# Performance work log

Measured on AMD Instinct MI355X. Metric: run time of the kernel, lower is better.

The kernel has to match this reference:

```python
import jax, jax.numpy as jnp
import numpy as np

D_MODEL = 1024
N_HEADS = 16
HEAD_DIM = D_MODEL // N_HEADS
WINDOW = 256


def setup_inputs() -> dict:
    key = jax.random.key(0)
    kx, kq, ko = jax.random.split(key, 3)
    B, T = 4, 2048
    x = jax.random.normal(kx, (B, T, D_MODEL), dtype=jnp.float32)
    s = 1.0 / np.sqrt(D_MODEL)
    w_qkv = jax.random.normal(kq, (D_MODEL, 3 * D_MODEL), dtype=jnp.float32) * s
    w_out = jax.random.normal(ko, (D_MODEL, D_MODEL), dtype=jnp.float32) * s
    return {"x": x, "w_qkv": w_qkv, "w_out": w_out}


def reference(x, w_qkv, w_out):
    B, T, C = x.shape
    qkv = (x @ w_qkv).reshape(B, T, 3, N_HEADS, HEAD_DIM)
    q, k, v = qkv[:, :, 0], qkv[:, :, 1], qkv[:, :, 2]  # [B,T,H,D]
    # sliding-window causal mask: position i attends to j in (i-W, i]
    i = jnp.arange(T)[:, None]
    j = jnp.arange(T)[None, :]
    allowed = (j <= i) & (j > i - WINDOW)
    mask = jnp.where(allowed, 0.0, -jnp.inf).astype(x.dtype)  # [T,T]
    scale = 1.0 / np.sqrt(HEAD_DIM)
    scores = jnp.einsum('bqhd,bkhd->bhqk', q, k) * scale + mask
    attn = jax.nn.softmax(scores, axis=-1)
    out = jnp.einsum('bhqk,bkhd->bqhd', attn, v).reshape(B, T, C)
    return out @ w_out
```

## Files before the change

### kernel.cpp

```cpp
#include <hip/hip_runtime.h>

typedef unsigned short u16;
typedef __attribute__((ext_vector_type(8))) short bh8;
typedef __attribute__((ext_vector_type(4))) float f4;
typedef __attribute__((ext_vector_type(4))) unsigned short us4;

#define T_SEQ 2048
#define NHEADS 16
#define DHEAD 64
#define WIN 256

__device__ __forceinline__ float bf2f(u16 u) {
  union { unsigned int i; float f; } v; v.i = ((unsigned int)u) << 16; return v.f;
}
__device__ __forceinline__ u16 f2bf(float f) {
  unsigned int u = __float_as_uint(f);
  u = u + 0x7fffu + ((u >> 16) & 1u);
  return (u16)(u >> 16);
}
__device__ __forceinline__ void async16(const void* g, void* l) {
  void* gv = const_cast<void*>(g);
  __builtin_amdgcn_global_load_lds(
      (__attribute__((address_space(1))) void*)gv,
      (__attribute__((address_space(3))) void*)l, 16, 0, 0);
}

__device__ __forceinline__ int is_f32_probe(const void* x) {
  const float* xf = (const float*)x;
  const int lane = threadIdx.x & 63;
  int bad = 0;
  #pragma unroll
  for (int u = 0; u < 4; ++u) {
    const float v = xf[lane * 4 + u];
    const float a = fabsf(v);
    bad |= (!(a < 64.f)) || (!(v == 0.f || a > 1e-30f));
  }
  return __any(bad) ? 0 : 1;
}

__global__ __launch_bounds__(256) void prep(
    const void* __restrict__ x, const void* __restrict__ w_qkv,
    const void* __restrict__ w_out, u16* __restrict__ xbf,
    u16* __restrict__ wqkvT, u16* __restrict__ woutT, int have_x)
{
  const int bid = blockIdx.x;
  const int tid = threadIdx.x;
  const int isf = is_f32_probe(x);

  if (bid < 4096) {
    if (!have_x) return;
    const size_t e = ((size_t)bid * 256 + tid) * 8;
    if (isf) {
      const float* f = (const float*)x;
      us4 o0, o1;
      #pragma unroll
      for (int u = 0; u < 4; ++u) { o0[u] = f2bf(f[e + u]); o1[u] = f2bf(f[e + 4 + u]); }
      *(us4*)&xbf[e] = o0; *(us4*)&xbf[e + 4] = o1;
    } else {
      *(us4*)&xbf[e]     = *(const us4*)&((const u16*)x)[e];
      *(us4*)&xbf[e + 4] = *(const us4*)&((const u16*)x)[e + 4];
    }
  } else {
    __shared__ alignas(16) u16 tile[32][33];
    const void* in; u16* out; int C, bx, by;
    if (bid < 4096 + 3072) { const int t = bid - 4096; in = w_qkv; out = wqkvT; C = 3072; bx = t % 96; by = t / 96; }
    else                   { const int t = bid - 7168; in = w_out; out = woutT; C = 1024; bx = t % 32; by = t / 32; }
    const int R = 1024;
    const int tx = tid & 31, ty = tid >> 5;
    const int xg = bx * 32 + tx;
    const int y0 = by * 32;
    #pragma unroll
    for (int i = ty; i < 32; i += 8) {
      u16 v;
      if (isf) v = f2bf(((const float*)in)[(size_t)(y0 + i) * C + xg]);
      else     v = ((const u16*)in)[(size_t)(y0 + i) * C + xg];
      tile[i][tx] = v;
    }
    __syncthreads();
    const int ox  = y0 + tx;
    const int oy0 = bx * 32;
    #pragma unroll
    for (int i = ty; i < 32; i += 8)
      out[(size_t)(oy0 + i) * R + ox] = tile[tx][i];
  }
}

template<bool ADYN, bool CDYN>
__global__ __launch_bounds__(256, 4) void gemm_bt(
    const void* __restrict__ A, const u16* __restrict__ Bt,
    void* __restrict__ C, int N, int K, int lda, int ldc,
    const void* __restrict__ xprobe)
{
  __shared__ alignas(16) u16 As[128 * 64];
  __shared__ alignas(16) u16 Bs[128 * 64];

  const int isf  = (ADYN || CDYN) ? is_f32_probe(xprobe) : 0;
  const int tid  = threadIdx.x;
  const int lane = tid & 63;
  const int w    = tid >> 6;
  const int wm   = (w >> 1) * 64;
  const int wn   = (w & 1) * 64;
  const int quad = lane >> 4;
  const int l16  = lane & 15;
  const int row0 = blockIdx.y * 128;
  const int col0 = blockIdx.x * 128;

  f4 acc[4][4] = {};

  size_t aoff[4]; const u16* bsrc[4]; int lofs[4];
  #pragma unroll
  for (int s = 0; s < 4; ++s) {
    const int r  = s * 32 + (tid >> 3);
    const int gc = (tid & 7) ^ (r & 7);
    aoff[s] = (size_t)(row0 + r) * lda + gc * 8;
    bsrc[s] = Bt + (size_t)(col0 + r) * K + gc * 8;
    lofs[s] = s * 4096 + tid * 16;
  }

  const bool af32 = ADYN && isf;

  for (int k0 = 0; k0 < K; k0 += 64) {
    if (af32) {
      const float* Af = (const float*)A;
      bh8 a[4];
      #pragma unroll
      for (int s = 0; s < 4; ++s) {
        f4 u0 = *(const f4*)(Af + aoff[s] + k0);
        f4 u1 = *(const f4*)(Af + aoff[s] + k0 + 4);
        #pragma unroll
        for (int u = 0; u < 4; ++u) { a[s][u] = (short)f2bf(u0[u]); a[s][u + 4] = (short)f2bf(u1[u]); }
      }
      __syncthreads();
      #pragma unroll
      for (int s = 0; s < 4; ++s) {
        *(bh8*)((char*)As + lofs[s]) = a[s];
        async16(bsrc[s] + k0, (char*)Bs + lofs[s]);
      }
    } else {
      const u16* A16 = (const u16*)A;
      __syncthreads();
      #pragma unroll
      for (int s = 0; s < 4; ++s) {
        async16(A16 + aoff[s] + k0, (char*)As + lofs[s]);
        async16(bsrc[s] + k0,       (char*)Bs + lofs[s]);
      }
    }
    __builtin_amdgcn_s_waitcnt(0);
    __syncthreads();

    #pragma unroll
    for (int ks = 0; ks < 2; ++ks) {
      bh8 af[4], bf[4];
      #pragma unroll
      for (int i = 0; i < 4; ++i) {
        const int row = wm + i * 16 + l16;
        const int lc  = (ks * 4 + quad) ^ (row & 7);
        af[i] = *(const bh8*)(As + row * 64 + lc * 8);
      }
      #pragma unroll
      for (int j = 0; j < 4; ++j) {
        const int row = wn + j * 16 + l16;
        const int lc  = (ks * 4 + quad) ^ (row & 7);
        bf[j] = *(const bh8*)(Bs + row * 64 + lc * 8);
      }
      #pragma unroll
      for (int i = 0; i < 4; ++i)
        #pragma unroll
        for (int j = 0; j < 4; ++j)
          acc[i][j] = __builtin_amdgcn_mfma_f32_16x16x32_bf16(af[i], bf[j], acc[i][j], 0, 0, 0);
    }
  }

  const bool cf32 = CDYN && isf;
  #pragma unroll
  for (int i = 0; i < 4; ++i) {
    #pragma unroll
    for (int j = 0; j < 4; ++j) {
      const int rb = row0 + wm + i * 16 + quad * 4;
      const int cc = col0 + wn + j * 16 + l16;
      #pragma unroll
      for (int r = 0; r < 4; ++r) {
        if (cf32) ((float*)C)[(size_t)(rb + r) * ldc + cc] = acc[i][j][r];
        else      ((u16*)C)[(size_t)(rb + r) * ldc + cc]   = f2bf(acc[i][j][r]);
      }
    }
  }
}

__global__ __launch_bounds__(256) void attn_mfma(const u16* __restrict__ qkv,
                                                 u16* __restrict__ att, int ldo)
{
  __shared__ alignas(16) u16 Kt[64 * 72];
  __shared__ alignas(16) u16 Vt[64 * 72];
  __shared__ alignas(16) u16 Ps[64 * 72];

  const int tid  = threadIdx.x;
  const int lane = tid & 63;
  const int w    = tid >> 6;
  const int quad = lane >> 4;
  const int l16  = lane & 15;
  const int qb = blockIdx.x, h = blockIdx.y, b = blockIdx.z;
  const int qs = qb * 64;

  const u16* base = qkv + (size_t)b * T_SEQ * 3072 + h * 64;

  const size_t qrowg = (size_t)(qs + w * 16 + l16) * 3072;
  bh8 qa0 = *(const bh8*)&base[qrowg + quad * 8];
  bh8 qa1 = *(const bh8*)&base[qrowg + 32 + quad * 8];
  #pragma unroll
  for (int u = 0; u < 8; ++u) {
    qa0[u] = (short)f2bf(bf2f((u16)qa0[u]) * 0.125f);
    qa1[u] = (short)f2bf(bf2f((u16)qa1[u]) * 0.125f);
  }

  f4 Oc[4] = {};
  float mst[4] = {-1e30f, -1e30f, -1e30f, -1e30f};
  float lst[4] = {0.f, 0.f, 0.f, 0.f};

  const int tmin = (qb >= 4) ? 0 : (4 - qb);
  const int c8  = (tid & 7) * 8;
  const int r0s = tid >> 3;

  for (int t = tmin; t < 5; ++t) {
    const int kt0 = qs - 256 + t * 64;
    const bool diag  = (t == 4);
    const bool ledge = (t == 0);
    const int kb_lo = ledge ? w : 0;
    const int kb_hi = diag  ? w : 3;
    __syncthreads();

    #pragma unroll
    for (int r = r0s; r < 64; r += 32) {
      *(bh8*)&Kt[r * 72 + c8] =
          *(const bh8*)&base[(size_t)(kt0 + r) * 3072 + 1024 + c8];
      bh8 v = *(const bh8*)&base[(size_t)(kt0 + r) * 3072 + 2048 + c8];
      const int kc = r >> 3, ki = r & 7;
      #pragma unroll
      for (int u = 0; u < 8; ++u) {
        const int d = c8 + u;
        Vt[d * 72 + ((kc ^ (d >> 3)) << 3) + ki] = (u16)v[u];
      }
    }
    __syncthreads();

    f4 S[4];
    #pragma unroll
    for (int kb = 0; kb < 4; ++kb) {
      if (kb < kb_lo || kb > kb_hi) {
        S[kb][0] = S[kb][1] = S[kb][2] = S[kb][3] = -1e30f;
      } else {
        const int krow = (kb * 16 + l16) * 72;
        bh8 kf0 = *(const bh8*)&Kt[krow + quad * 8];
        bh8 kf1 = *(const bh8*)&Kt[krow + 32 + quad * 8];
        f4 s = {};
        s = __builtin_amdgcn_mfma_f32_16x16x32_bf16(qa0, kf0, s, 0, 0, 0);
        s = __builtin_amdgcn_mfma_f32_16x16x32_bf16(qa1, kf1, s, 0, 0, 0);
        S[kb] = s;
      }
    }

    if (diag || ledge) {
      #pragma unroll
      for (int kb = 0; kb < 4; ++kb) {
        if (kb == w) {
          #pragma unroll
          for (int rr = 0; rr < 4; ++rr) {
            const int ii = quad * 4 + rr;
            const bool ok = diag ? (l16 <= ii) : (l16 > ii);
            if (!ok) S[kb][rr] = -1e30f;
          }
        }
      }
    }

    float tmax[4] = {-1e30f, -1e30f, -1e30f, -1e30f};
    #pragma unroll
    for (int kb = 0; kb < 4; ++kb)
      #pragma unroll
      for (int rr = 0; rr < 4; ++rr)
        tmax[rr] = fmaxf(tmax[rr], S[kb][rr]);
    #pragma unroll
    for (int off = 1; off < 16; off <<= 1)
      #pragma unroll
      for (int rr = 0; rr < 4; ++rr)
        tmax[rr] = fmaxf(tmax[rr], __shfl_xor(tmax[rr], off));

    const bool grew = (tmax[0] > mst[0] + 8.f) || (tmax[1] > mst[1] + 8.f) ||
                      (tmax[2] > mst[2] + 8.f) || (tmax[3] > mst[3] + 8.f);
    if (__any(grew)) {
      #pragma unroll
      for (int rr = 0; rr < 4; ++rr) {
        const float mnew = fmaxf(mst[rr], tmax[rr]);
        const float al = __expf(mst[rr] - mnew);
        mst[rr] = mnew;
        lst[rr] *= al;
        #pragma unroll
        for (int db = 0; db < 4; ++db) Oc[db][rr] *= al;
      }
    }

    float rsum[4] = {0.f, 0.f, 0.f, 0.f};
    const int swq = quad >> 1;
    #pragma unroll
    for (int kb = 0; kb < 4; ++kb) {
      const int kc = kb * 2 + (l16 >> 3);
      const int ki = l16 & 7;
      #pragma unroll
      for (int rr = 0; rr < 4; ++rr) {
        const float p = __expf(S[kb][rr] - mst[rr]);
        rsum[rr] += p;
        const int q = w * 16 + quad * 4 + rr;
        Ps[q * 72 + ((kc ^ swq) << 3) + ki] = f2bf(p);
      }
    }
    #pragma unroll
    for (int off = 1; off < 16; off <<= 1)
      #pragma unroll
      for (int rr = 0; rr < 4; ++rr)
        rsum[rr] += __shfl_xor(rsum[rr], off);
    #pragma unroll
    for (int rr = 0; rr < 4; ++rr)
      lst[rr] += rsum[rr];

    {
      const int q = w * 16 + l16;
      const int sw = (q >> 3) & 1;
      bh8 pa0 = *(const bh8*)&Ps[q * 72 + (((0 + quad) ^ sw) << 3)];
      bh8 pa1 = *(const bh8*)&Ps[q * 72 + (((4 + quad) ^ sw) << 3)];
      #pragma unroll
      for (int db = 0; db < 4; ++db) {
        const int d = db * 16 + l16;
        const int dsw = d >> 3;
        bh8 vb0 = *(const bh8*)&Vt[d * 72 + (((0 + quad) ^ dsw) << 3)];
        bh8 vb1 = *(const bh8*)&Vt[d * 72 + (((4 + quad) ^ dsw) << 3)];
        Oc[db] = __builtin_amdgcn_mfma_f32_16x16x32_bf16(pa0, vb0, Oc[db], 0, 0, 0);
        Oc[db] = __builtin_amdgcn_mfma_f32_16x16x32_bf16(pa1, vb1, Oc[db], 0, 0, 0);
      }
    }
  }

  u16* obase = att + (size_t)b * T_SEQ * ldo + h * 64;
  #pragma unroll
  for (int rr = 0; rr < 4; ++rr) {
    const int i = qs + w * 16 + quad * 4 + rr;
    const float inv = 1.f / lst[rr];
    #pragma unroll
    for (int db = 0; db < 4; ++db)
      obase[(size_t)i * ldo + db * 16 + l16] = f2bf(Oc[db][rr] * inv);
  }
}

extern "C" void kernel_launch(void* const* d_in, const int* in_sizes, int n_in,
                              void* d_out, int out_size, void* d_ws, size_t ws_size,
                              hipStream_t stream) {
  const void* x     = d_in[0];
  const void* w_qkv = d_in[1];
  const void* w_out = d_in[2];

  const size_t SZ_QKV = (size_t)8192 * 3072 * 2;
  const size_t SZ_XBF = (size_t)8192 * 1024 * 2;
  const size_t SZ_WQ  = (size_t)3072 * 1024 * 2;
  const size_t SZ_WO  = (size_t)1024 * 1024 * 2;
  const size_t SZ_ATT = (size_t)8192 * 1024 * 2;

  char* p = (char*)d_ws;
  u16* qkv   = (u16*)p; p += SZ_QKV;
  u16* wqkvT = (u16*)p; p += SZ_WQ;
  u16* woutT = (u16*)p; p += SZ_WO;
  u16* xbf   = (u16*)p; p += SZ_XBF;
  u16* attb  = (u16*)p;
  const size_t need_x   = SZ_QKV + SZ_WQ + SZ_WO + SZ_XBF;
  const bool have_x   = ws_size >= need_x;
  const bool have_att = ws_size >= need_x + SZ_ATT;

  prep<<<dim3(8192), 256, 0, stream>>>(x, w_qkv, w_out, xbf, wqkvT, woutT,
                                       have_x ? 1 : 0);

  if (have_x) {
    gemm_bt<false, false><<<dim3(24, 64), 256, 0, stream>>>(
        xbf, wqkvT, qkv, 3072, 1024, 1024, 3072, x);
  } else {
    gemm_bt<true, false><<<dim3(24, 64), 256, 0, stream>>>(
        x, wqkvT, qkv, 3072, 1024, 1024, 3072, x);
  }

  u16* attp  = have_att ? attb : qkv;
  const int ldo = have_att ? 1024 : 3072;
  attn_mfma<<<dim3(32, NHEADS, 4), 256, 0, stream>>>(qkv, attp, ldo);

  gemm_bt<false, true><<<dim3(8, 64), 256, 0, stream>>>(
      attp, woutT, d_out, 1024, 1024, ldo, 1024, x);
}
```

Measured before the change: 226.6 us.

## Add single-pass windowed attention kernel with pre-transposed V and GEMM tile swizzle

```diff
diff --git a/kernel.cpp b/kernel.cpp
--- a/kernel.cpp
+++ b/kernel.cpp
@@ -9,6 +9,8 @@
 #define NHEADS 16
 #define DHEAD 64
 #define WIN 256
+
+#define MF(a, b, c) __builtin_amdgcn_mfma_f32_16x16x32_bf16((a), (b), (c), 0, 0, 0)
 
 __device__ __forceinline__ float bf2f(u16 u) {
   union { unsigned int i; float f; } v; v.i = ((unsigned int)u) << 16; return v.f;
@@ -102,8 +104,18 @@
   const int wn   = (w & 1) * 64;
   const int quad = lane >> 4;
   const int l16  = lane & 15;
-  const int row0 = blockIdx.y * 128;
-  const int col0 = blockIdx.x * 128;
+
+  int bx = blockIdx.x, by = blockIdx.y;
+  {
+    const int nx = gridDim.x, nwg = nx * gridDim.y;
+    if ((nwg & 7) == 0) {
+      const int lin = by * nx + bx;
+      const int sw  = (lin & 7) * (nwg >> 3) + (lin >> 3);
+      bx = sw % nx; by = sw / nx;
+    }
+  }
+  const int row0 = by * 128;
+  const int col0 = bx * 128;
 
   f4 acc[4][4] = {};
 
@@ -167,7 +179,7 @@
       for (int i = 0; i < 4; ++i)
         #pragma unroll
         for (int j = 0; j < 4; ++j)
-          acc[i][j] = __builtin_amdgcn_mfma_f32_16x16x32_bf16(af[i], bf[j], acc[i][j], 0, 0, 0);
+          acc[i][j] = MF(af[i], bf[j], acc[i][j]);
     }
   }
 
@@ -184,6 +196,169 @@
         else      ((u16*)C)[(size_t)(rb + r) * ldc + cc]   = f2bf(acc[i][j][r]);
       }
     }
+  }
+}
+
+__global__ __launch_bounds__(256) void vtrans(const u16* __restrict__ qkv,
+                                              u16* __restrict__ vT)
+{
+  __shared__ alignas(16) u16 tile[32][33];
+  const int tid = threadIdx.x;
+  const int bh = blockIdx.z;
+  const int b = bh >> 4, h = bh & 15;
+  const int k0 = blockIdx.x * 32, d0 = blockIdx.y * 32;
+  const int tx = tid & 31, ty = tid >> 5;
+  const u16* src = qkv + (size_t)b * T_SEQ * 3072 + 2048 + h * 64;
+  #pragma unroll
+  for (int i = ty; i < 32; i += 8)
+    tile[i][tx] = src[(size_t)(k0 + i) * 3072 + d0 + tx];
+  __syncthreads();
+  u16* dst = vT + ((size_t)bh * 64 + d0) * T_SEQ + k0;
+  #pragma unroll
+  for (int i = ty; i < 32; i += 8)
+    dst[(size_t)i * T_SEQ + tx] = tile[tx][i];
+}
+
+__global__ __launch_bounds__(512) void attn_win(const u16* __restrict__ qkv,
+                                                const u16* __restrict__ vT,
+                                                u16* __restrict__ att, int ldo)
+{
+  __shared__ alignas(16) u16 Kt[384 * 64];
+  __shared__ alignas(16) u16 Vt[64 * 384];
+  __shared__ alignas(16) u16 Ps[8 * 16 * 72];
+
+  const int tid  = threadIdx.x;
+  const int lane = tid & 63;
+  const int w    = tid >> 6;
+  const int quad = lane >> 4;
+  const int l16  = lane & 15;
+  const int qb = blockIdx.x, h = blockIdx.y, b = blockIdx.z;
+  const int qs = qb * 128;
+  const int kbase = qs - 256;
+
+  const u16* base = qkv + (size_t)b * T_SEQ * 3072 + h * 64;
+  const u16* vTbh = vT + (size_t)(b * NHEADS + h) * 64 * T_SEQ;
+
+  #pragma unroll
+  for (int s = 0; s < 6; ++s) {
+    const int id = s * 512 + tid;
+    const int r  = id >> 3;
+    const int gc = (id & 7) ^ (r & 7);
+    int gk = kbase + r; gk = gk < 0 ? 0 : gk;
+    async16(&base[(size_t)gk * 3072 + 1024 + gc * 8], (char*)Kt + id * 16);
+  }
+  #pragma unroll
+  for (int s = 0; s < 6; ++s) {
+    const int id = s * 512 + tid;
+    const int d  = id / 48;
+    const int c  = id - d * 48;
+    const int gc = c ^ (d & 7);
+    int gk = kbase + gc * 8; gk = gk < 0 ? 0 : gk;
+    async16(vTbh + (size_t)d * T_SEQ + gk, (char*)Vt + id * 16);
+  }
+
+  const int q0w = qs + w * 16;
+  const size_t qrowg = (size_t)(q0w + l16) * 3072;
+  bh8 qa0 = *(const bh8*)&base[qrowg + quad * 8];
+  bh8 qa1 = *(const bh8*)&base[qrowg + 32 + quad * 8];
+  #pragma unroll
+  for (int u = 0; u < 8; ++u) {
+    qa0[u] = (short)f2bf(bf2f((u16)qa0[u]) * 0.125f);
+    qa1[u] = (short)f2bf(bf2f((u16)qa1[u]) * 0.125f);
+  }
+
+  __builtin_amdgcn_s_waitcnt(0);
+  __syncthreads();
+
+  const int qw16 = (qs >> 4) + w;
+  const int t_lo = qw16 >= 16 ? 0 : 16 - qw16;
+  const bool has_ledge = (t_lo == 0);
+
+  f4 S[17];
+  __builtin_amdgcn_s_setprio(1);
+  #pragma unroll
+  for (int t = 0; t < 17; ++t) {
+    if (t >= t_lo) {
+      const int kr = 16 * (w + t) + l16;
+      const int sw = l16 & 7;
+      bh8 kf0 = *(const bh8*)&Kt[kr * 64 + ((quad    ) ^ sw) * 8];
+      bh8 kf1 = *(const bh8*)&Kt[kr * 64 + ((quad + 4) ^ sw) * 8];
+      f4 s = {};
+      s = MF(qa0, kf0, s);
+      s = MF(qa1, kf1, s);
+      S[t] = s;
+    }
+  }
+  __builtin_amdgcn_s_setprio(0);
+
+  #pragma unroll
+  for (int rr = 0; rr < 4; ++rr) {
+    const int ii = quad * 4 + rr;
+    if (l16 > ii) S[16][rr] = -1e30f;
+    if (has_ledge && l16 <= ii) S[0][rr] = -1e30f;
+  }
+
+  float rsum[4] = {0.f, 0.f, 0.f, 0.f};
+  #pragma unroll
+  for (int t = 0; t < 17; ++t) {
+    if (t >= t_lo) {
+      #pragma unroll
+      for (int rr = 0; rr < 4; ++rr) {
+        const float p = __expf(S[t][rr]);
+        S[t][rr] = p;
+        rsum[rr] += p;
+      }
+    }
+  }
+  #pragma unroll
+  for (int off = 1; off < 16; off <<= 1)
+    #pragma unroll
+    for (int rr = 0; rr < 4; ++rr)
+      rsum[rr] += __shfl_xor(rsum[rr], off);
+
+  u16* Psw = Ps + w * 16 * 72;
+  f4 Oc[4] = {};
+  const int swq = quad >> 1;
+  const int swp = (l16 >> 3) & 1;
+  #pragma unroll
+  for (int g = 0; g < 5; ++g) {
+    if (4 * g + 3 < t_lo && g != 4) continue;
+    #pragma unroll
+    for (int kb = 0; kb < 4; ++kb) {
+      const int t = 4 * g + kb;
+      const int kc = kb * 2 + (l16 >> 3);
+      const int ki = l16 & 7;
+      #pragma unroll
+      for (int rr = 0; rr < 4; ++rr) {
+        const int qloc = quad * 4 + rr;
+        const u16 pv = (t <= 16 && t >= t_lo) ? f2bf(S[t][rr]) : (u16)0;
+        Psw[qloc * 72 + ((kc ^ swq) << 3) + ki] = pv;
+      }
+    }
+    bh8 pa0 = *(const bh8*)&Psw[l16 * 72 + (((0 + quad) ^ swp) << 3)];
+    bh8 pa1 = *(const bh8*)&Psw[l16 * 72 + (((4 + quad) ^ swp) << 3)];
+    __builtin_amdgcn_s_setprio(1);
+    #pragma unroll
+    for (int db = 0; db < 4; ++db) {
+      const int d = db * 16 + l16;
+      int cc0 = 2 * w + 8 * g + quad;     cc0 = cc0 > 47 ? 47 : cc0;
+      int cc1 = 2 * w + 8 * g + quad + 4; cc1 = cc1 > 47 ? 47 : cc1;
+      bh8 vb0 = *(const bh8*)&Vt[d * 384 + (cc0 ^ (d & 7)) * 8];
+      bh8 vb1 = *(const bh8*)&Vt[d * 384 + (cc1 ^ (d & 7)) * 8];
+      Oc[db] = MF(pa0, vb0, Oc[db]);
+      Oc[db] = MF(pa1, vb1, Oc[db]);
+    }
+    __builtin_amdgcn_s_setprio(0);
+  }
+
+  u16* obase = att + (size_t)b * T_SEQ * ldo + h * 64;
+  #pragma unroll
+  for (int rr = 0; rr < 4; ++rr) {
+    const int i = q0w + quad * 4 + rr;
+    const float inv = 1.f / rsum[rr];
+    #pragma unroll
+    for (int db = 0; db < 4; ++db)
+      obase[(size_t)i * ldo + db * 16 + l16] = f2bf(Oc[db][rr] * inv);
   }
 }
 
@@ -253,8 +428,8 @@
         bh8 kf0 = *(const bh8*)&Kt[krow + quad * 8];
         bh8 kf1 = *(const bh8*)&Kt[krow + 32 + quad * 8];
         f4 s = {};
-        s = __builtin_amdgcn_mfma_f32_16x16x32_bf16(qa0, kf0, s, 0, 0, 0);
-        s = __builtin_amdgcn_mfma_f32_16x16x32_bf16(qa1, kf1, s, 0, 0, 0);
+        s = MF(qa0, kf0, s);
+        s = MF(qa1, kf1, s);
         S[kb] = s;
       }
     }
@@ -324,17 +499,17 @@
 
     {
       const int q = w * 16 + l16;
-      const int sw = (q >> 3) & 1;
-      bh8 pa0 = *(const bh8*)&Ps[q * 72 + (((0 + quad) ^ sw) << 3)];
-      bh8 pa1 = *(const bh8*)&Ps[q * 72 + (((4 + quad) ^ sw) << 3)];
+      const int swp = (q >> 3) & 1;
+      bh8 pa0 = *(const bh8*)&Ps[q * 72 + (((0 + quad) ^ swp) << 3)];
+      bh8 pa1 = *(const bh8*)&Ps[q * 72 + (((4 + quad) ^ swp) << 3)];
       #pragma unroll
       for (int db = 0; db < 4; ++db) {
         const int d = db * 16 + l16;
         const int dsw = d >> 3;
         bh8 vb0 = *(const bh8*)&Vt[d * 72 + (((0 + quad) ^ dsw) << 3)];
         bh8 vb1 = *(const bh8*)&Vt[d * 72 + (((4 + quad) ^ dsw) << 3)];
-        Oc[db] = __builtin_amdgcn_mfma_f32_16x16x32_bf16(pa0, vb0, Oc[db], 0, 0, 0);
-        Oc[db] = __builtin_amdgcn_mfma_f32_16x16x32_bf16(pa1, vb1, Oc[db], 0, 0, 0);
+        Oc[db] = MF(pa0, vb0, Oc[db]);
+        Oc[db] = MF(pa1, vb1, Oc[db]);
       }
     }
   }
@@ -361,6 +536,7 @@
   const size_t SZ_XBF = (size_t)8192 * 1024 * 2;
   const size_t SZ_WQ  = (size_t)3072 * 1024 * 2;
   const size_t SZ_WO  = (size_t)1024 * 1024 * 2;
+  const size_t SZ_VT  = (size_t)64 * 64 * 2048 * 2;
   const size_t SZ_ATT = (size_t)8192 * 1024 * 2;
 
   char* p = (char*)d_ws;
@@ -368,10 +544,12 @@
   u16* wqkvT = (u16*)p; p += SZ_WQ;
   u16* woutT = (u16*)p; p += SZ_WO;
   u16* xbf   = (u16*)p; p += SZ_XBF;
+  u16* vTb   = (u16*)p; p += SZ_VT;
   u16* attb  = (u16*)p;
-  const size_t need_x   = SZ_QKV + SZ_WQ + SZ_WO + SZ_XBF;
-  const bool have_x   = ws_size >= need_x;
-  const bool have_att = ws_size >= need_x + SZ_ATT;
+  const size_t need_x  = SZ_QKV + SZ_WQ + SZ_WO + SZ_XBF;
+  const bool have_x    = ws_size >= need_x;
+  const bool have_vt   = ws_size >= need_x + SZ_VT;
+  const bool have_att  = ws_size >= need_x + SZ_VT + SZ_ATT;
 
   prep<<<dim3(8192), 256, 0, stream>>>(x, w_qkv, w_out, xbf, wqkvT, woutT,
                                        have_x ? 1 : 0);
@@ -384,9 +562,14 @@
         x, wqkvT, qkv, 3072, 1024, 1024, 3072, x);
   }
 
-  u16* attp  = have_att ? attb : qkv;
+  u16* attp = have_att ? attb : qkv;
   const int ldo = have_att ? 1024 : 3072;
-  attn_mfma<<<dim3(32, NHEADS, 4), 256, 0, stream>>>(qkv, attp, ldo);
+  if (have_vt) {
+    vtrans<<<dim3(64, 2, 64), 256, 0, stream>>>(qkv, vTb);
+    attn_win<<<dim3(16, NHEADS, 4), 512, 0, stream>>>(qkv, vTb, attp, ldo);
+  } else {
+    attn_mfma<<<dim3(32, NHEADS, 4), 256, 0, stream>>>(qkv, attp, ldo);
+  }
 
   gemm_bt<false, true><<<dim3(8, 64), 256, 0, stream>>>(
       attp, woutT, d_out, 1024, 1024, ldo, 1024, x);
```

After: 232.3 us. 1.03x slower.

## Fuse all stages into one persistent kernel with grid barriers

Applied to the files above, without the earlier changes.

```diff
diff --git a/kernel.cpp b/kernel.cpp
--- a/kernel.cpp
+++ b/kernel.cpp
@@ -9,6 +9,9 @@
 #define NHEADS 16
 #define DHEAD 64
 #define WIN 256
+#define NBLK 512
+
+#define MF(a, b, c) __builtin_amdgcn_mfma_f32_16x16x32_bf16((a), (b), (c), 0, 0, 0)
 
 __device__ __forceinline__ float bf2f(u16 u) {
   union { unsigned int i; float f; } v; v.i = ((unsigned int)u) << 16; return v.f;
@@ -36,6 +39,327 @@
     bad |= (!(a < 64.f)) || (!(v == 0.f || a > 1e-30f));
   }
   return __any(bad) ? 0 : 1;
+}
+
+__device__ __forceinline__ void gridbar(unsigned int* bar, unsigned int target) {
+  __syncthreads();
+  if (threadIdx.x == 0) {
+    __hip_atomic_fetch_add(bar, 1u, __ATOMIC_ACQ_REL, __HIP_MEMORY_SCOPE_AGENT);
+    while (__hip_atomic_load(bar, __ATOMIC_ACQUIRE, __HIP_MEMORY_SCOPE_AGENT) < target) {
+      __builtin_amdgcn_s_sleep(8);
+    }
+  }
+  __syncthreads();
+  __threadfence();
+}
+
+__device__ __forceinline__ void gtile(
+    const u16* __restrict__ A, const u16* __restrict__ Bt, void* __restrict__ C,
+    int K, int lda, int ldc, int row0, int col0, bool cf32,
+    u16* As, u16* Bs)
+{
+  const int tid  = threadIdx.x;
+  const int lane = tid & 63;
+  const int w    = tid >> 6;
+  const int wm   = (w >> 1) * 64;
+  const int wn   = (w & 1) * 64;
+  const int quad = lane >> 4;
+  const int l16  = lane & 15;
+
+  f4 acc[4][4] = {};
+
+  size_t aoff[4]; const u16* bsrc[4]; int lofs[4];
+  #pragma unroll
+  for (int s = 0; s < 4; ++s) {
+    const int r  = s * 32 + (tid >> 3);
+    const int gc = (tid & 7) ^ (r & 7);
+    aoff[s] = (size_t)(row0 + r) * lda + gc * 8;
+    bsrc[s] = Bt + (size_t)(col0 + r) * K + gc * 8;
+    lofs[s] = s * 4096 + tid * 16;
+  }
+
+  for (int k0 = 0; k0 < K; k0 += 64) {
+    __syncthreads();
+    #pragma unroll
+    for (int s = 0; s < 4; ++s) {
+      async16(A + aoff[s] + k0, (char*)As + lofs[s]);
+      async16(bsrc[s] + k0,     (char*)Bs + lofs[s]);
+    }
+    __builtin_amdgcn_s_waitcnt(0);
+    __syncthreads();
+
+    #pragma unroll
+    for (int ks = 0; ks < 2; ++ks) {
+      bh8 af[4], bf[4];
+      #pragma unroll
+      for (int i = 0; i < 4; ++i) {
+        const int row = wm + i * 16 + l16;
+        const int lc  = (ks * 4 + quad) ^ (row & 7);
+        af[i] = *(const bh8*)(As + row * 64 + lc * 8);
+      }
+      #pragma unroll
+      for (int j = 0; j < 4; ++j) {
+        const int row = wn + j * 16 + l16;
+        const int lc  = (ks * 4 + quad) ^ (row & 7);
+        bf[j] = *(const bh8*)(Bs + row * 64 + lc * 8);
+      }
+      #pragma unroll
+      for (int i = 0; i < 4; ++i)
+        #pragma unroll
+        for (int j = 0; j < 4; ++j)
+          acc[i][j] = MF(af[i], bf[j], acc[i][j]);
+    }
+  }
+  __syncthreads();
+
+  #pragma unroll
+  for (int i = 0; i < 4; ++i) {
+    #pragma unroll
+    for (int j = 0; j < 4; ++j) {
+      const int rb = row0 + wm + i * 16 + quad * 4;
+      const int cc = col0 + wn + j * 16 + l16;
+      #pragma unroll
+      for (int r = 0; r < 4; ++r) {
+        if (cf32) ((float*)C)[(size_t)(rb + r) * ldc + cc] = acc[i][j][r];
+        else      ((u16*)C)[(size_t)(rb + r) * ldc + cc]   = f2bf(acc[i][j][r]);
+      }
+    }
+  }
+}
+
+__device__ __forceinline__ void attn_vb(
+    const u16* __restrict__ qkv, u16* __restrict__ att, int ldo,
+    int qb, int h, int b, u16* Kt, u16* Vt, u16* Ps)
+{
+  const int tid  = threadIdx.x;
+  const int lane = tid & 63;
+  const int w    = tid >> 6;
+  const int quad = lane >> 4;
+  const int l16  = lane & 15;
+  const int qs = qb * 64;
+
+  const u16* base = qkv + (size_t)b * T_SEQ * 3072 + h * 64;
+
+  const size_t qrowg = (size_t)(qs + w * 16 + l16) * 3072;
+  bh8 qa0 = *(const bh8*)&base[qrowg + quad * 8];
+  bh8 qa1 = *(const bh8*)&base[qrowg + 32 + quad * 8];
+  #pragma unroll
+  for (int u = 0; u < 8; ++u) {
+    qa0[u] = (short)f2bf(bf2f((u16)qa0[u]) * 0.125f);
+    qa1[u] = (short)f2bf(bf2f((u16)qa1[u]) * 0.125f);
+  }
+
+  f4 Oc[4] = {};
+  float mst[4] = {-1e30f, -1e30f, -1e30f, -1e30f};
+  float lst[4] = {0.f, 0.f, 0.f, 0.f};
+
+  const int tmin = (qb >= 4) ? 0 : (4 - qb);
+  const int c8  = (tid & 7) * 8;
+  const int r0s = tid >> 3;
+
+  for (int t = tmin; t < 5; ++t) {
+    const int kt0 = qs - 256 + t * 64;
+    const bool diag  = (t == 4);
+    const bool ledge = (t == 0);
+    const int kb_lo = ledge ? w : 0;
+    const int kb_hi = diag  ? w : 3;
+    __syncthreads();
+
+    #pragma unroll
+    for (int r = r0s; r < 64; r += 32) {
+      *(bh8*)&Kt[r * 72 + c8] =
+          *(const bh8*)&base[(size_t)(kt0 + r) * 3072 + 1024 + c8];
+      bh8 v = *(const bh8*)&base[(size_t)(kt0 + r) * 3072 + 2048 + c8];
+      const int kc = r >> 3, ki = r & 7;
+      #pragma unroll
+      for (int u = 0; u < 8; ++u) {
+        const int d = c8 + u;
+        Vt[d * 72 + ((kc ^ (d >> 3)) << 3) + ki] = (u16)v[u];
+      }
+    }
+    __syncthreads();
+
+    f4 S[4];
+    #pragma unroll
+    for (int kb = 0; kb < 4; ++kb) {
+      if (kb < kb_lo || kb > kb_hi) {
+        S[kb][0] = S[kb][1] = S[kb][2] = S[kb][3] = -1e30f;
+      } else {
+        const int krow = (kb * 16 + l16) * 72;
+        bh8 kf0 = *(const bh8*)&Kt[krow + quad * 8];
+        bh8 kf1 = *(const bh8*)&Kt[krow + 32 + quad * 8];
+        f4 s = {};
+        s = MF(qa0, kf0, s);
+        s = MF(qa1, kf1, s);
+        S[kb] = s;
+      }
+    }
+
+    if (diag || ledge) {
+      #pragma unroll
+      for (int kb = 0; kb < 4; ++kb) {
+        if (kb == w) {
+          #pragma unroll
+          for (int rr = 0; rr < 4; ++rr) {
+            const int ii = quad * 4 + rr;
+            const bool ok = diag ? (l16 <= ii) : (l16 > ii);
+            if (!ok) S[kb][rr] = -1e30f;
+          }
+        }
+      }
+    }
+
+    float tmax[4] = {-1e30f, -1e30f, -1e30f, -1e30f};
+    #pragma unroll
+    for (int kb = 0; kb < 4; ++kb)
+      #pragma unroll
+      for (int rr = 0; rr < 4; ++rr)
+        tmax[rr] = fmaxf(tmax[rr], S[kb][rr]);
+    #pragma unroll
+    for (int off = 1; off < 16; off <<= 1)
+      #pragma unroll
+      for (int rr = 0; rr < 4; ++rr)
+        tmax[rr] = fmaxf(tmax[rr], __shfl_xor(tmax[rr], off));
+
+    const bool grew = (tmax[0] > mst[0] + 8.f) || (tmax[1] > mst[1] + 8.f) ||
+                      (tmax[2] > mst[2] + 8.f) || (tmax[3] > mst[3] + 8.f);
+    if (__any(grew)) {
+      #pragma unroll
+      for (int rr = 0; rr < 4; ++rr) {
+        const float mnew = fmaxf(mst[rr], tmax[rr]);
+        const float al = __expf(mst[rr] - mnew);
+        mst[rr] = mnew;
+        lst[rr] *= al;
+        #pragma unroll
+        for (int db = 0; db < 4; ++db) Oc[db][rr] *= al;
+      }
+    }
+
+    float rsum[4] = {0.f, 0.f, 0.f, 0.f};
+    const int swq = quad >> 1;
+    #pragma unroll
+    for (int kb = 0; kb < 4; ++kb) {
+      const int kc = kb * 2 + (l16 >> 3);
+      const int ki = l16 & 7;
+      #pragma unroll
+      for (int rr = 0; rr < 4; ++rr) {
+        const float p = __expf(S[kb][rr] - mst[rr]);
+        rsum[rr] += p;
+        const int q = w * 16 + quad * 4 + rr;
+        Ps[q * 72 + ((kc ^ swq) << 3) + ki] = f2bf(p);
+      }
+    }
+    #pragma unroll
+    for (int off = 1; off < 16; off <<= 1)
+      #pragma unroll
+      for (int rr = 0; rr < 4; ++rr)
+        rsum[rr] += __shfl_xor(rsum[rr], off);
+    #pragma unroll
+    for (int rr = 0; rr < 4; ++rr)
+      lst[rr] += rsum[rr];
+
+    {
+      const int q = w * 16 + l16;
+      const int swp = (q >> 3) & 1;
+      bh8 pa0 = *(const bh8*)&Ps[q * 72 + (((0 + quad) ^ swp) << 3)];
+      bh8 pa1 = *(const bh8*)&Ps[q * 72 + (((4 + quad) ^ swp) << 3)];
+      #pragma unroll
+      for (int db = 0; db < 4; ++db) {
+        const int d = db * 16 + l16;
+        const int dsw = d >> 3;
+        bh8 vb0 = *(const bh8*)&Vt[d * 72 + (((0 + quad) ^ dsw) << 3)];
+        bh8 vb1 = *(const bh8*)&Vt[d * 72 + (((4 + quad) ^ dsw) << 3)];
+        Oc[db] = MF(pa0, vb0, Oc[db]);
+        Oc[db] = MF(pa1, vb1, Oc[db]);
+      }
+    }
+  }
+  __syncthreads();
+
+  u16* obase = att + (size_t)b * T_SEQ * ldo + h * 64;
+  #pragma unroll
+  for (int rr = 0; rr < 4; ++rr) {
+    const int i = qs + w * 16 + quad * 4 + rr;
+    const float inv = 1.f / lst[rr];
+    #pragma unroll
+    for (int db = 0; db < 4; ++db)
+      obase[(size_t)i * ldo + db * 16 + l16] = f2bf(Oc[db][rr] * inv);
+  }
+}
+
+__global__ __launch_bounds__(256, 2) void fused(
+    const void* __restrict__ x, const void* __restrict__ w_qkv,
+    const void* __restrict__ w_out, void* __restrict__ out,
+    u16* __restrict__ xbf, u16* __restrict__ wqkvT, u16* __restrict__ woutT,
+    u16* __restrict__ qkv, u16* __restrict__ attb, unsigned int* bar)
+{
+  __shared__ alignas(16) u16 smem[2 * 128 * 64];
+  const int bid = blockIdx.x;
+  const int tid = threadIdx.x;
+  const int isf = is_f32_probe(x);
+
+  #pragma unroll
+  for (int i = 0; i < 8; ++i) {
+    const size_t e = (((size_t)(bid * 8 + i)) * 256 + tid) * 8;
+    if (isf) {
+      const float* f = (const float*)x;
+      us4 o0, o1;
+      #pragma unroll
+      for (int u = 0; u < 4; ++u) { o0[u] = f2bf(f[e + u]); o1[u] = f2bf(f[e + 4 + u]); }
+      *(us4*)&xbf[e] = o0; *(us4*)&xbf[e + 4] = o1;
+    } else {
+      *(us4*)&xbf[e]     = *(const us4*)&((const u16*)x)[e];
+      *(us4*)&xbf[e + 4] = *(const us4*)&((const u16*)x)[e + 4];
+    }
+  }
+  {
+    u16 (*tile)[33] = (u16(*)[33])smem;
+    const int tx4 = (tid & 7) * 4;
+    const int iy  = tid >> 3;
+    for (int i = 0; i < 8; ++i) {
+      const int j = bid * 8 + i;
+      const void* in; u16* outw; int C, bx, by;
+      if (j < 3072) { in = w_qkv; outw = wqkvT; C = 3072; bx = j % 96; by = j / 96; }
+      else          { const int t = j - 3072; in = w_out; outw = woutT; C = 1024; bx = t % 32; by = t / 32; }
+      const int y0 = by * 32;
+      __syncthreads();
+      if (isf) {
+        f4 v = *(const f4*)&((const float*)in)[(size_t)(y0 + iy) * C + bx * 32 + tx4];
+        #pragma unroll
+        for (int u = 0; u < 4; ++u) tile[iy][tx4 + u] = f2bf(v[u]);
+      } else {
+        us4 v = *(const us4*)&((const u16*)in)[(size_t)(y0 + iy) * C + bx * 32 + tx4];
+        #pragma unroll
+        for (int u = 0; u < 4; ++u) tile[iy][tx4 + u] = v[u];
+      }
+      __syncthreads();
+      const int i2 = tid >> 3;
+      us4 o;
+      #pragma unroll
+      for (int u = 0; u < 4; ++u) o[u] = tile[tx4 + u][i2];
+      *(us4*)&outw[(size_t)(bx * 32 + i2) * 1024 + y0 + tx4] = o;
+    }
+  }
+  gridbar(bar, NBLK);
+
+  #pragma unroll
+  for (int i = 0; i < 3; ++i) {
+    const int t = bid + NBLK * i;
+    gtile(xbf, wqkvT, qkv, 1024, 1024, 3072,
+          (t / 24) * 128, (t % 24) * 128, false, smem, smem + 8192);
+  }
+  gridbar(bar, 2 * NBLK);
+
+  #pragma unroll
+  for (int i = 0; i < 4; ++i) {
+    const int t = bid + NBLK * i;
+    attn_vb(qkv, attb, 1024, t & 31, (t >> 5) & 15, t >> 9,
+            smem, smem + 4608, smem + 9216);
+  }
+  gridbar(bar, 3 * NBLK);
+
+  gtile(attb, woutT, out, 1024, 1024, 1024,
+        (bid / 8) * 128, (bid % 8) * 128, isf != 0, smem, smem + 8192);
 }
 
 __global__ __launch_bounds__(256) void prep(
@@ -65,23 +389,24 @@
     const void* in; u16* out; int C, bx, by;
     if (bid < 4096 + 3072) { const int t = bid - 4096; in = w_qkv; out = wqkvT; C = 3072; bx = t % 96; by = t / 96; }
     else                   { const int t = bid - 7168; in = w_out; out = woutT; C = 1024; bx = t % 32; by = t / 32; }
-    const int R = 1024;
-    const int tx = tid & 31, ty = tid >> 5;
-    const int xg = bx * 32 + tx;
+    const int tx4 = (tid & 7) * 4;
+    const int iy  = tid >> 3;
     const int y0 = by * 32;
-    #pragma unroll
-    for (int i = ty; i < 32; i += 8) {
-      u16 v;
-      if (isf) v = f2bf(((const float*)in)[(size_t)(y0 + i) * C + xg]);
-      else     v = ((const u16*)in)[(size_t)(y0 + i) * C + xg];
-      tile[i][tx] = v;
+    if (isf) {
+      f4 v = *(const f4*)&((const float*)in)[(size_t)(y0 + iy) * C + bx * 32 + tx4];
+      #pragma unroll
+      for (int u = 0; u < 4; ++u) tile[iy][tx4 + u] = f2bf(v[u]);
+    } else {
+      us4 v = *(const us4*)&((const u16*)in)[(size_t)(y0 + iy) * C + bx * 32 + tx4];
+      #pragma unroll
+      for (int u = 0; u < 4; ++u) tile[iy][tx4 + u] = v[u];
     }
     __syncthreads();
-    const int ox  = y0 + tx;
-    const int oy0 = bx * 32;
-    #pragma unroll
-    for (int i = ty; i < 32; i += 8)
-      out[(size_t)(oy0 + i) * R + ox] = tile[tx][i];
+    const int i2 = tid >> 3;
+    us4 o;
+    #pragma unroll
+    for (int u = 0; u < 4; ++u) o[u] = tile[tx4 + u][i2];
+    *(us4*)&out[(size_t)(bx * 32 + i2) * 1024 + y0 + tx4] = o;
   }
 }
 
@@ -167,7 +492,7 @@
       for (int i = 0; i < 4; ++i)
         #pragma unroll
         for (int j = 0; j < 4; ++j)
-          acc[i][j] = __builtin_amdgcn_mfma_f32_16x16x32_bf16(af[i], bf[j], acc[i][j], 0, 0, 0);
+          acc[i][j] = MF(af[i], bf[j], acc[i][j]);
     }
   }
 
@@ -187,167 +512,13 @@
   }
 }
 
-__global__ __launch_bounds__(256) void attn_mfma(const u16* __restrict__ qkv,
-                                                 u16* __restrict__ att, int ldo)
+__global__ __launch_bounds__(256) void attn_legacy(const u16* __restrict__ qkv,
+                                                   u16* __restrict__ att, int ldo)
 {
   __shared__ alignas(16) u16 Kt[64 * 72];
   __shared__ alignas(16) u16 Vt[64 * 72];
   __shared__ alignas(16) u16 Ps[64 * 72];
-
-  const int tid  = threadIdx.x;
-  const int lane = tid & 63;
-  const int w    = tid >> 6;
-  const int quad = lane >> 4;
-  const int l16  = lane & 15;
-  const int qb = blockIdx.x, h = blockIdx.y, b = blockIdx.z;
-  const int qs = qb * 64;
-
-  const u16* base = qkv + (size_t)b * T_SEQ * 3072 + h * 64;
-
-  const size_t qrowg = (size_t)(qs + w * 16 + l16) * 3072;
-  bh8 qa0 = *(const bh8*)&base[qrowg + quad * 8];
-  bh8 qa1 = *(const bh8*)&base[qrowg + 32 + quad * 8];
-  #pragma unroll
-  for (int u = 0; u < 8; ++u) {
-    qa0[u] = (short)f2bf(bf2f((u16)qa0[u]) * 0.125f);
-    qa1[u] = (short)f2bf(bf2f((u16)qa1[u]) * 0.125f);
-  }
-
-  f4 Oc[4] = {};
-  float mst[4] = {-1e30f, -1e30f, -1e30f, -1e30f};
-  float lst[4] = {0.f, 0.f, 0.f, 0.f};
-
-  const int tmin = (qb >= 4) ? 0 : (4 - qb);
-  const int c8  = (tid & 7) * 8;
-  const int r0s = tid >> 3;
-
-  for (int t = tmin; t < 5; ++t) {
-    const int kt0 = qs - 256 + t * 64;
-    const bool diag  = (t == 4);
-    const bool ledge = (t == 0);
-    const int kb_lo = ledge ? w : 0;
-    const int kb_hi = diag  ? w : 3;
-    __syncthreads();
-
-    #pragma unroll
-    for (int r = r0s; r < 64; r += 32) {
-      *(bh8*)&Kt[r * 72 + c8] =
-          *(const bh8*)&base[(size_t)(kt0 + r) * 3072 + 1024 + c8];
-      bh8 v = *(const bh8*)&base[(size_t)(kt0 + r) * 3072 + 2048 + c8];
-      const int kc = r >> 3, ki = r & 7;
-      #pragma unroll
-      for (int u = 0; u < 8; ++u) {
-        const int d = c8 + u;
-        Vt[d * 72 + ((kc ^ (d >> 3)) << 3) + ki] = (u16)v[u];
-      }
-    }
-    __syncthreads();
-
-    f4 S[4];
-    #pragma unroll
-    for (int kb = 0; kb < 4; ++kb) {
-      if (kb < kb_lo || kb > kb_hi) {
-        S[kb][0] = S[kb][1] = S[kb][2] = S[kb][3] = -1e30f;
-      } else {
-        const int krow = (kb * 16 + l16) * 72;
-        bh8 kf0 = *(const bh8*)&Kt[krow + quad * 8];
-        bh8 kf1 = *(const bh8*)&Kt[krow + 32 + quad * 8];
-        f4 s = {};
-        s = __builtin_amdgcn_mfma_f32_16x16x32_bf16(qa0, kf0, s, 0, 0, 0);
-        s = __builtin_amdgcn_mfma_f32_16x16x32_bf16(qa1, kf1, s, 0, 0, 0);
-        S[kb] = s;
-      }
-    }
-
-    if (diag || ledge) {
-      #pragma unroll
-      for (int kb = 0; kb < 4; ++kb) {
-        if (kb == w) {
-          #pragma unroll
-          for (int rr = 0; rr < 4; ++rr) {
-            const int ii = quad * 4 + rr;
-            const bool ok = diag ? (l16 <= ii) : (l16 > ii);
-            if (!ok) S[kb][rr] = -1e30f;
-          }
-        }
-      }
-    }
-
-    float tmax[4] = {-1e30f, -1e30f, -1e30f, -1e30f};
-    #pragma unroll
-    for (int kb = 0; kb < 4; ++kb)
-      #pragma unroll
-      for (int rr = 0; rr < 4; ++rr)
-        tmax[rr] = fmaxf(tmax[rr], S[kb][rr]);
-    #pragma unroll
-    for (int off = 1; off < 16; off <<= 1)
-      #pragma unroll
-      for (int rr = 0; rr < 4; ++rr)
-        tmax[rr] = fmaxf(tmax[rr], __shfl_xor(tmax[rr], off));
-
-    const bool grew = (tmax[0] > mst[0] + 8.f) || (tmax[1] > mst[1] + 8.f) ||
-                      (tmax[2] > mst[2] + 8.f) || (tmax[3] > mst[3] + 8.f);
-    if (__any(grew)) {
-      #pragma unroll
-      for (int rr = 0; rr < 4; ++rr) {
-        const float mnew = fmaxf(mst[rr], tmax[rr]);
-        const float al = __expf(mst[rr] - mnew);
-        mst[rr] = mnew;
-        lst[rr] *= al;
-        #pragma unroll
-        for (int db = 0; db < 4; ++db) Oc[db][rr] *= al;
-      }
-    }
-
-    float rsum[4] = {0.f, 0.f, 0.f, 0.f};
-    const int swq = quad >> 1;
-    #pragma unroll
-    for (int kb = 0; kb < 4; ++kb) {
-      const int kc = kb * 2 + (l16 >> 3);
-      const int ki = l16 & 7;
-      #pragma unroll
-      for (int rr = 0; rr < 4; ++rr) {
-        const float p = __expf(S[kb][rr] - mst[rr]);
-        rsum[rr] += p;
-        const int q = w * 16 + quad * 4 + rr;
-        Ps[q * 72 + ((kc ^ swq) << 3) + ki] = f2bf(p);
-      }
-    }
-    #pragma unroll
-    for (int off = 1; off < 16; off <<= 1)
-      #pragma unroll
-      for (int rr = 0; rr < 4; ++rr)
-        rsum[rr] += __shfl_xor(rsum[rr], off);
-    #pragma unroll
-    for (int rr = 0; rr < 4; ++rr)
-      lst[rr] += rsum[rr];
-
-    {
-      const int q = w * 16 + l16;
-      const int sw = (q >> 3) & 1;
-      bh8 pa0 = *(const bh8*)&Ps[q * 72 + (((0 + quad) ^ sw) << 3)];
-      bh8 pa1 = *(const bh8*)&Ps[q * 72 + (((4 + quad) ^ sw) << 3)];
-      #pragma unroll
-      for (int db = 0; db < 4; ++db) {
-        const int d = db * 16 + l16;
-        const int dsw = d >> 3;
-        bh8 vb0 = *(const bh8*)&Vt[d * 72 + (((0 + quad) ^ dsw) << 3)];
-        bh8 vb1 = *(const bh8*)&Vt[d * 72 + (((4 + quad) ^ dsw) << 3)];
-        Oc[db] = __builtin_amdgcn_mfma_f32_16x16x32_bf16(pa0, vb0, Oc[db], 0, 0, 0);
-        Oc[db] = __builtin_amdgcn_mfma_f32_16x16x32_bf16(pa1, vb1, Oc[db], 0, 0, 0);
-      }
-    }
-  }
-
-  u16* obase = att + (size_t)b * T_SEQ * ldo + h * 64;
-  #pragma unroll
-  for (int rr = 0; rr < 4; ++rr) {
-    const int i = qs + w * 16 + quad * 4 + rr;
-    const float inv = 1.f / lst[rr];
-    #pragma unroll
-    for (int db = 0; db < 4; ++db)
-      obase[(size_t)i * ldo + db * 16 + l16] = f2bf(Oc[db][rr] * inv);
-  }
+  attn_vb(qkv, att, ldo, blockIdx.x, blockIdx.y, blockIdx.z, Kt, Vt, Ps);
 }
 
 extern "C" void kernel_launch(void* const* d_in, const int* in_sizes, int n_in,
@@ -368,14 +539,24 @@
   u16* wqkvT = (u16*)p; p += SZ_WQ;
   u16* woutT = (u16*)p; p += SZ_WO;
   u16* xbf   = (u16*)p; p += SZ_XBF;
-  u16* attb  = (u16*)p;
-  const size_t need_x   = SZ_QKV + SZ_WQ + SZ_WO + SZ_XBF;
-  const bool have_x   = ws_size >= need_x;
-  const bool have_att = ws_size >= need_x + SZ_ATT;
+  u16* attb  = (u16*)p; p += SZ_ATT;
+  unsigned int* bar = (unsigned int*)p; p += 256;
+
+  const size_t need_x     = SZ_QKV + SZ_WQ + SZ_WO + SZ_XBF;
+  const size_t need_fused = need_x + SZ_ATT + 256;
+  const bool have_x     = ws_size >= need_x;
+  const bool have_att   = ws_size >= need_x + SZ_ATT;
+  const bool have_fused = ws_size >= need_fused;
+
+  if (have_fused) {
+    hipMemsetAsync(bar, 0, 64, stream);
+    fused<<<dim3(NBLK), 256, 0, stream>>>(
+        x, w_qkv, w_out, d_out, xbf, wqkvT, woutT, qkv, attb, bar);
+    return;
+  }
 
   prep<<<dim3(8192), 256, 0, stream>>>(x, w_qkv, w_out, xbf, wqkvT, woutT,
                                        have_x ? 1 : 0);
-
   if (have_x) {
     gemm_bt<false, false><<<dim3(24, 64), 256, 0, stream>>>(
         xbf, wqkvT, qkv, 3072, 1024, 1024, 3072, x);
@@ -383,11 +564,9 @@
     gemm_bt<true, false><<<dim3(24, 64), 256, 0, stream>>>(
         x, wqkvT, qkv, 3072, 1024, 1024, 3072, x);
   }
-
-  u16* attp  = have_att ? attb : qkv;
+  u16* attp = have_att ? attb : qkv;
   const int ldo = have_att ? 1024 : 3072;
-  attn_mfma<<<dim3(32, NHEADS, 4), 256, 0, stream>>>(qkv, attp, ldo);
-
+  attn_legacy<<<dim3(32, NHEADS, 4), 256, 0, stream>>>(qkv, attp, ldo);
   gemm_bt<false, true><<<dim3(8, 64), 256, 0, stream>>>(
       attp, woutT, d_out, 1024, 1024, ldo, 1024, x);
 }
```

Result: slower. 541.9 us (+139.2%).

## Fuse x fp32-to-bf16 conversion into QKV GEMM and vectorize weight transpose

Applied to the files above, without the earlier changes.

```diff
diff --git a/kernel.cpp b/kernel.cpp
--- a/kernel.cpp
+++ b/kernel.cpp
@@ -9,6 +9,8 @@
 #define NHEADS 16
 #define DHEAD 64
 #define WIN 256
+
+#define MF(a, b, c) __builtin_amdgcn_mfma_f32_16x16x32_bf16((a), (b), (c), 0, 0, 0)
 
 __device__ __forceinline__ float bf2f(u16 u) {
   union { unsigned int i; float f; } v; v.i = ((unsigned int)u) << 16; return v.f;
@@ -40,49 +42,35 @@
 
 __global__ __launch_bounds__(256) void prep(
     const void* __restrict__ x, const void* __restrict__ w_qkv,
-    const void* __restrict__ w_out, u16* __restrict__ xbf,
-    u16* __restrict__ wqkvT, u16* __restrict__ woutT, int have_x)
+    const void* __restrict__ w_out, u16* __restrict__ wqkvT,
+    u16* __restrict__ woutT)
 {
   const int bid = blockIdx.x;
   const int tid = threadIdx.x;
   const int isf = is_f32_probe(x);
 
-  if (bid < 4096) {
-    if (!have_x) return;
-    const size_t e = ((size_t)bid * 256 + tid) * 8;
-    if (isf) {
-      const float* f = (const float*)x;
-      us4 o0, o1;
-      #pragma unroll
-      for (int u = 0; u < 4; ++u) { o0[u] = f2bf(f[e + u]); o1[u] = f2bf(f[e + 4 + u]); }
-      *(us4*)&xbf[e] = o0; *(us4*)&xbf[e + 4] = o1;
-    } else {
-      *(us4*)&xbf[e]     = *(const us4*)&((const u16*)x)[e];
-      *(us4*)&xbf[e + 4] = *(const us4*)&((const u16*)x)[e + 4];
-    }
+  __shared__ alignas(16) u16 tile[32][33];
+  const void* in; u16* out; int C, bx, by;
+  if (bid < 3072) { in = w_qkv; out = wqkvT; C = 3072; bx = bid % 96; by = bid / 96; }
+  else            { const int t = bid - 3072; in = w_out; out = woutT; C = 1024; bx = t % 32; by = t / 32; }
+  const int tx4 = (tid & 7) * 4;
+  const int iy  = tid >> 3;
+  const int y0 = by * 32;
+  if (isf) {
+    f4 v = *(const f4*)&((const float*)in)[(size_t)(y0 + iy) * C + bx * 32 + tx4];
+    #pragma unroll
+    for (int u = 0; u < 4; ++u) tile[iy][tx4 + u] = f2bf(v[u]);
   } else {
-    __shared__ alignas(16) u16 tile[32][33];
-    const void* in; u16* out; int C, bx, by;
-    if (bid < 4096 + 3072) { const int t = bid - 4096; in = w_qkv; out = wqkvT; C = 3072; bx = t % 96; by = t / 96; }
-    else                   { const int t = bid - 7168; in = w_out; out = woutT; C = 1024; bx = t % 32; by = t / 32; }
-    const int R = 1024;
-    const int tx = tid & 31, ty = tid >> 5;
-    const int xg = bx * 32 + tx;
-    const int y0 = by * 32;
-    #pragma unroll
-    for (int i = ty; i < 32; i += 8) {
-      u16 v;
-      if (isf) v = f2bf(((const float*)in)[(size_t)(y0 + i) * C + xg]);
-      else     v = ((const u16*)in)[(size_t)(y0 + i) * C + xg];
-      tile[i][tx] = v;
-    }
-    __syncthreads();
-    const int ox  = y0 + tx;
-    const int oy0 = bx * 32;
-    #pragma unroll
-    for (int i = ty; i < 32; i += 8)
-      out[(size_t)(oy0 + i) * R + ox] = tile[tx][i];
-  }
+    us4 v = *(const us4*)&((const u16*)in)[(size_t)(y0 + iy) * C + bx * 32 + tx4];
+    #pragma unroll
+    for (int u = 0; u < 4; ++u) tile[iy][tx4 + u] = v[u];
+  }
+  __syncthreads();
+  const int i2 = tid >> 3;
+  us4 o;
+  #pragma unroll
+  for (int u = 0; u < 4; ++u) o[u] = tile[tx4 + u][i2];
+  *(us4*)&out[(size_t)(bx * 32 + i2) * 1024 + y0 + tx4] = o;
 }
 
 template<bool ADYN, bool CDYN>
@@ -167,7 +155,7 @@
       for (int i = 0; i < 4; ++i)
         #pragma unroll
         for (int j = 0; j < 4; ++j)
-          acc[i][j] = __builtin_amdgcn_mfma_f32_16x16x32_bf16(af[i], bf[j], acc[i][j], 0, 0, 0);
+          acc[i][j] = MF(af[i], bf[j], acc[i][j]);
     }
   }
 
@@ -253,8 +241,8 @@
         bh8 kf0 = *(const bh8*)&Kt[krow + quad * 8];
         bh8 kf1 = *(const bh8*)&Kt[krow + 32 + quad * 8];
         f4 s = {};
-        s = __builtin_amdgcn_mfma_f32_16x16x32_bf16(qa0, kf0, s, 0, 0, 0);
-        s = __builtin_amdgcn_mfma_f32_16x16x32_bf16(qa1, kf1, s, 0, 0, 0);
+        s = MF(qa0, kf0, s);
+        s = MF(qa1, kf1, s);
         S[kb] = s;
       }
     }
@@ -324,17 +312,17 @@
 
     {
       const int q = w * 16 + l16;
-      const int sw = (q >> 3) & 1;
-      bh8 pa0 = *(const bh8*)&Ps[q * 72 + (((0 + quad) ^ sw) << 3)];
-      bh8 pa1 = *(const bh8*)&Ps[q * 72 + (((4 + quad) ^ sw) << 3)];
+      const int swp = (q >> 3) & 1;
+      bh8 pa0 = *(const bh8*)&Ps[q * 72 + (((0 + quad) ^ swp) << 3)];
+      bh8 pa1 = *(const bh8*)&Ps[q * 72 + (((4 + quad) ^ swp) << 3)];
       #pragma unroll
       for (int db = 0; db < 4; ++db) {
         const int d = db * 16 + l16;
         const int dsw = d >> 3;
         bh8 vb0 = *(const bh8*)&Vt[d * 72 + (((0 + quad) ^ dsw) << 3)];
         bh8 vb1 = *(const bh8*)&Vt[d * 72 + (((4 + quad) ^ dsw) << 3)];
-        Oc[db] = __builtin_amdgcn_mfma_f32_16x16x32_bf16(pa0, vb0, Oc[db], 0, 0, 0);
-        Oc[db] = __builtin_amdgcn_mfma_f32_16x16x32_bf16(pa1, vb1, Oc[db], 0, 0, 0);
+        Oc[db] = MF(pa0, vb0, Oc[db]);
+        Oc[db] = MF(pa1, vb1, Oc[db]);
       }
     }
   }
@@ -358,7 +346,6 @@
   const void* w_out = d_in[2];
 
   const size_t SZ_QKV = (size_t)8192 * 3072 * 2;
-  const size_t SZ_XBF = (size_t)8192 * 1024 * 2;
   const size_t SZ_WQ  = (size_t)3072 * 1024 * 2;
   const size_t SZ_WO  = (size_t)1024 * 1024 * 2;
   const size_t SZ_ATT = (size_t)8192 * 1024 * 2;
@@ -367,22 +354,14 @@
   u16* qkv   = (u16*)p; p += SZ_QKV;
   u16* wqkvT = (u16*)p; p += SZ_WQ;
   u16* woutT = (u16*)p; p += SZ_WO;
-  u16* xbf   = (u16*)p; p += SZ_XBF;
   u16* attb  = (u16*)p;
-  const size_t need_x   = SZ_QKV + SZ_WQ + SZ_WO + SZ_XBF;
-  const bool have_x   = ws_size >= need_x;
-  const bool have_att = ws_size >= need_x + SZ_ATT;
-
-  prep<<<dim3(8192), 256, 0, stream>>>(x, w_qkv, w_out, xbf, wqkvT, woutT,
-                                       have_x ? 1 : 0);
-
-  if (have_x) {
-    gemm_bt<false, false><<<dim3(24, 64), 256, 0, stream>>>(
-        xbf, wqkvT, qkv, 3072, 1024, 1024, 3072, x);
-  } else {
-    gemm_bt<true, false><<<dim3(24, 64), 256, 0, stream>>>(
-        x, wqkvT, qkv, 3072, 1024, 1024, 3072, x);
-  }
+  const size_t need     = SZ_QKV + SZ_WQ + SZ_WO;
+  const bool have_att   = ws_size >= need + SZ_ATT;
+
+  prep<<<dim3(4096), 256, 0, stream>>>(x, w_qkv, w_out, wqkvT, woutT);
+
+  gemm_bt<true, false><<<dim3(24, 64), 256, 0, stream>>>(
+      x, wqkvT, qkv, 3072, 1024, 1024, 3072, x);
 
   u16* attp  = have_att ? attb : qkv;
   const int ldo = have_att ? 1024 : 3072;
```

Measured after the change: 302.5 us. 33.5% more time.
